# Kernel optimization log

Measured on AMD Instinct MI355X. Metric: run time of the kernel, lower is better.

Reference implementation:

```python
import jax, jax.numpy as jnp
import numpy as np

B, Q, K, D, H = 4, 2048, 2048, 512, 8
DH = D // H
MASK_VAL = -1e6


def setup_inputs() -> dict:
    key = jax.random.key(0)
    ks = jax.random.split(key, 8)
    queries = jax.random.normal(ks[0], (B, Q, D), dtype=jnp.float32)
    keys = jax.random.normal(ks[1], (B, K, D), dtype=jnp.float32)
    values = jax.random.normal(ks[2], (B, K, D), dtype=jnp.float32)
    valid_lens = jax.random.randint(ks[3], (B,), 1, K + 1, dtype=jnp.int32)
    # torch nn.Linear weights: shape [out_features, in_features], y = x @ W.T
    s = 1.0 / np.sqrt(D)
    W_q = jax.random.uniform(ks[4], (D, D), jnp.float32, -s, s)
    W_k = jax.random.uniform(ks[5], (D, D), jnp.float32, -s, s)
    W_v = jax.random.uniform(ks[6], (D, D), jnp.float32, -s, s)
    W_o = jax.random.uniform(ks[7], (D, D), jnp.float32, -s, s)
    return {"queries": queries, "keys": keys, "values": values,
            "valid_lens": valid_lens, "W_q": W_q, "W_k": W_k,
            "W_v": W_v, "W_o": W_o}


def _split_heads(x):
    # [B, S, D] -> [B, H, S, DH]
    b, s, _ = x.shape
    return x.reshape(b, s, H, DH).transpose(0, 2, 1, 3)


def reference(queries, keys, values, valid_lens, W_q, W_k, W_v, W_o):
    q = _split_heads(queries @ W_q.T)   # [B,H,Q,DH]
    k = _split_heads(keys @ W_k.T)      # [B,H,K,DH]
    v = _split_heads(values @ W_v.T)    # [B,H,K,DH]
    scores = jnp.einsum("bhqd,bhkd->bhqk", q, k) / jnp.sqrt(jnp.float32(DH))
    # padding mask: key position < valid_len[b], broadcast over heads & queries
    mask = jnp.arange(K)[None, None, None, :] < valid_lens[:, None, None, None]
    scores = jnp.where(mask, scores, MASK_VAL)
    attn = jax.nn.softmax(scores, axis=-1)  # dropout=eval/no-op
    out = jnp.einsum("bhqk,bhkd->bhqd", attn, v)
    out = out.transpose(0, 2, 1, 3).reshape(queries.shape[0], q.shape[2], D)
    return out @ W_o.T
```

## Files before the change

### kernel.cpp

```cpp
#include <hip/hip_runtime.h>
#include <cstdint>
#include <cstddef>

#define BB  4
#define QQ  2048
#define SK  2048
#define DD  512
#define HH  8
#define DHH 64
#define CS  16
#define ZMAX 2

typedef __bf16 bf16;
typedef bf16  bf16x8 __attribute__((ext_vector_type(8)));
typedef bf16  bf16x4 __attribute__((ext_vector_type(4)));
typedef float f32x4  __attribute__((ext_vector_type(4)));
typedef uint32_t u32x4 __attribute__((ext_vector_type(4)));
typedef _Float16 f16;
typedef f16   f16x4 __attribute__((ext_vector_type(4)));
typedef f16   f16x8 __attribute__((ext_vector_type(8)));

__device__ __forceinline__ void async16(void* lds, const void* g) {
  __builtin_amdgcn_global_load_lds(
      (const __attribute__((address_space(1))) unsigned int*)g,
      (__attribute__((address_space(3))) unsigned int*)lds, 16, 0, 0);
}

__device__ __forceinline__ uint32_t pk2(float lo, float hi) {
  return __builtin_amdgcn_perm(__builtin_bit_cast(uint32_t, hi),
                               __builtin_bit_cast(uint32_t, lo), 0x07060302u);
}

__global__ __launch_bounds__(256) void cvt_all(
    const float* __restrict__ q, const float* __restrict__ k,
    const float* __restrict__ v, const float* __restrict__ w0,
    const float* __restrict__ w1, const float* __restrict__ w2,
    const float* __restrict__ w3, bf16* __restrict__ dq,
    bf16* __restrict__ dk, bf16* __restrict__ dv, bf16* __restrict__ dw0,
    bf16* __restrict__ dw1, bf16* __restrict__ dw2, bf16* __restrict__ dw3,
    int nx4, int nw4) {
  int i = blockIdx.x * 256 + threadIdx.x;
  const float* s;
  bf16* d;
  if (i < nx4)               { s = q;  d = dq;  }
  else if (i < 2 * nx4)      { s = k;  d = dk;  i -= nx4; }
  else if (i < 3 * nx4)      { s = v;  d = dv;  i -= 2 * nx4; }
  else {
    int j = i - 3 * nx4;
    if (j < nw4)             { s = w0; d = dw0; }
    else if (j < 2 * nw4)    { s = w1; d = dw1; j -= nw4; }
    else if (j < 3 * nw4)    { s = w2; d = dw2; j -= 2 * nw4; }
    else if (j < 4 * nw4)    { s = w3; d = dw3; j -= 3 * nw4; }
    else return;
    i = j;
  }
  float4 vv = ((const float4*)s)[i];
  bf16x4 o;
  o[0] = (bf16)vv.x; o[1] = (bf16)vv.y; o[2] = (bf16)vv.z; o[3] = (bf16)vv.w;
  ((bf16x4*)d)[i] = o;
}

template <int MT, typename EpiF>
__device__ __forceinline__ void gemm_body(
    const bf16* __restrict__ A, const bf16* __restrict__ B,
    int tM, int tN, EpiF epi_fn) {
  __shared__ __align__(16) bf16 lA[MT * 32 * 64];
  __shared__ __align__(16) bf16 lB[128 * 64];
  const int tid  = threadIdx.x;
  const int l    = tid & 63;
  const int w    = tid >> 6;
  const int lrow = l & 15, lq = l >> 4;
  const int wm = (w >> 1) * (MT * 16), wn = (w & 1) * 64;

  f32x4 acc[MT][4] = {};
  for (int it = 0; it < 8; ++it) {
    const int kt = it * 64;
    if (it) __syncthreads();
#pragma unroll
    for (int j = 0; j < MT; ++j) {
      int c = j * 256 + tid, row = c >> 3, gcc = (c & 7) ^ (row & 7);
      async16(&lA[c * 8], &A[(size_t)(tM + row) * DD + kt + gcc * 8]);
    }
#pragma unroll
    for (int j = 0; j < 4; ++j) {
      int c = j * 256 + tid, row = c >> 3, gcc = (c & 7) ^ (row & 7);
      async16(&lB[c * 8], &B[(size_t)(tN + row) * DD + kt + gcc * 8]);
    }
    __syncthreads();

#pragma unroll
    for (int ks = 0; ks < 2; ++ks) {
      bf16x8 af[MT], bfr[4];
#pragma unroll
      for (int mt = 0; mt < MT; ++mt) {
        int row = wm + mt * 16 + lrow;
        int chunk = row * 8 + ((ks * 4 + lq) ^ (lrow & 7));
        af[mt] = *(const bf16x8*)&lA[chunk * 8];
      }
#pragma unroll
      for (int nt = 0; nt < 4; ++nt) {
        int row = wn + nt * 16 + lrow;
        int chunk = row * 8 + ((ks * 4 + lq) ^ (lrow & 7));
        bfr[nt] = *(const bf16x8*)&lB[chunk * 8];
      }
#pragma unroll
      for (int mt = 0; mt < MT; ++mt)
#pragma unroll
        for (int nt = 0; nt < 4; ++nt)
          acc[mt][nt] = __builtin_amdgcn_mfma_f32_16x16x32_bf16(
              af[mt], bfr[nt], acc[mt][nt], 0, 0, 0);
    }
  }

#pragma unroll
  for (int mt = 0; mt < MT; ++mt)
#pragma unroll
    for (int nt = 0; nt < 4; ++nt) {
      int row0 = tM + wm + mt * 16 + lq * 4;
      int col  = tN + wn + nt * 16 + lrow;
      epi_fn(acc[mt][nt], row0, col);
    }
}

__global__ __launch_bounds__(256, 3) void proj3(
    const bf16* __restrict__ xq, const bf16* __restrict__ wq, bf16* __restrict__ qh,
    const bf16* __restrict__ xk, const bf16* __restrict__ wk, bf16* __restrict__ kh,
    const bf16* __restrict__ xv, const bf16* __restrict__ wv, bf16* __restrict__ vt,
    float qscale) {
  const int z = blockIdx.y, x = blockIdx.x;
  if (z < 2) {
    const bf16* A  = z == 0 ? wq : wk;
    const bf16* B  = z == 0 ? xq : xk;
    bf16* Cout     = z == 0 ? qh : kh;
    const float scale = z == 0 ? qscale : 1.0f;
    int tM = (x & 3) * 128, tN = (x >> 2) * 128;
    gemm_body<4>(A, B, tM, tN, [&](const f32x4& a, int row0, int col) {
      int b2 = col >> 11, s = col & 2047;
      int h2 = row0 >> 6, dh0 = row0 & 63;
      bf16x4 o;
#pragma unroll
      for (int r = 0; r < 4; ++r) o[r] = (bf16)(a[r] * scale);
      *(bf16x4*)&Cout[((size_t)(b2 * HH + h2) * QQ + s) * DHH + dh0] = o;
    });
  } else {
    int tM = (x >> 2) * 128, tN = (x & 3) * 128;
    gemm_body<4>(xv, wv, tM, tN, [&](const f32x4& a, int row0, int col) {
      int b2 = row0 >> 11, s0 = row0 & 2047;
      int h2 = col >> 6,  dh = col & 63;
      int tile = s0 >> 6, kk = s0 & 63;
      int g = kk >> 4, a2 = (kk >> 2) & 3;
      int idx0 = ((g >> 1) * 4 + a2) * 8 + (g & 1) * 4;
      bf16x4 o;
#pragma unroll
      for (int r = 0; r < 4; ++r) o[r] = (bf16)a[r];
      *(bf16x4*)&vt[((size_t)(b2 * HH + h2) * DHH + dh) * SK + tile * 64 + idx0] = o;
    });
  }
}

__global__ __launch_bounds__(256, 3) void proj_o(
    const bf16* __restrict__ wo, const bf16* __restrict__ ao,
    float* __restrict__ Cout) {
  const int x = blockIdx.x;
  int tM = (x & 7) * 64, tN = (x >> 3) * 128;
  gemm_body<2>(wo, ao, tM, tN, [&](const f32x4& a, int row0, int col) {
    *(float4*)&Cout[(size_t)col * DD + row0] = *(const float4*)&a;
  });
}

__global__ __launch_bounds__(256, 3) void attn_split(
    const bf16* __restrict__ qh, const bf16* __restrict__ kh,
    const bf16* __restrict__ vt, const int* __restrict__ valid_lens,
    f16* __restrict__ opart, float* __restrict__ lpart) {
  __shared__ __align__(16) bf16 lK[3][64 * 64];
  __shared__ __align__(16) bf16 lV[3][64 * 64];
  const int tid  = threadIdx.x;
  const int l    = tid & 63;
  const int w    = tid >> 6;
  const int lrow = l & 15, lq = l >> 4;
  const int rx   = lrow & 7;
  const int bh = blockIdx.x;
  const int b = bh >> 3;
  const int qt = blockIdx.y, z = blockIdx.z;
  const int vl  = valid_lens[b];
  const int nkt = (vl + 63) >> 6;
  const int kt0 = z * CS;
  const int kt1 = min(nkt, kt0 + CS);
  const size_t pbase = ((size_t)bh * 16 + qt) * ZMAX + z;
  float* lout = lpart + pbase * 128;
  f16*   oout = opart + pbase * 8192;

  if (kt0 >= kt1) {
    if (tid < 128) lout[tid] = 0.f;
    return;
  }

  const int q0 = qt * 128 + w * 32;
  const bf16* qbase = qh + (size_t)bh * QQ * DHH;
  const bf16* kbase = kh + (size_t)bh * SK * DHH;
  const bf16* vbase = vt + (size_t)bh * DHH * SK;

  auto stageKV = [&](int k0, int buf) {
#pragma unroll
    for (int j = 0; j < 2; ++j) {
      int c = j * 256 + tid, row = c >> 3, gcc = (c & 7) ^ (row & 7);
      async16(&lK[buf][c * 8], &kbase[(size_t)(k0 + row) * DHH + gcc * 8]);
    }
#pragma unroll
    for (int j = 0; j < 2; ++j) {
      int c = j * 256 + tid, row = c >> 3, gcc = (c & 7) ^ (row & 7);
      async16(&lV[buf][c * 8], &vbase[(size_t)row * SK + k0 + gcc * 8]);
    }
  };

  bf16x8 qf[2][2];
#pragma unroll
  for (int g = 0; g < 2; ++g)
#pragma unroll
    for (int ks = 0; ks < 2; ++ks)
      qf[g][ks] = *(const bf16x8*)
          &qbase[(size_t)(q0 + g * 16 + lrow) * DHH + ks * 32 + lq * 8];

  f32x4 acc[2][4] = {};
  float rs[2] = {0.f, 0.f};

  stageKV(kt0 * 64, 0);
  asm volatile("s_waitcnt vmcnt(0)" ::: "memory");

  for (int kt = kt0; kt < kt1; ++kt) {
    const int bi = (kt - kt0) % 3;
    if (kt + 1 < kt1) {
      stageKV((kt + 1) * 64, (kt + 1 - kt0) % 3);
      asm volatile("s_waitcnt vmcnt(4)" ::: "memory");
    } else {
      asm volatile("s_waitcnt vmcnt(0)" ::: "memory");
    }
    __builtin_amdgcn_s_barrier();
    asm volatile("" ::: "memory");
    const bf16* bufK = lK[bi];
    const bf16* bufV = lV[bi];
    const int k0 = kt * 64;

    f32x4 s[2][4] = {};
#pragma unroll
    for (int ks = 0; ks < 2; ++ks) {
#pragma unroll
      for (int t = 0; t < 4; ++t) {
        int row = t * 16 + lrow;
        int chunkc = row * 8 + ((ks * 4 + lq) ^ rx);
        bf16x8 kf = *(const bf16x8*)&bufK[chunkc * 8];
#pragma unroll
        for (int g = 0; g < 2; ++g)
          s[g][t] = __builtin_amdgcn_mfma_f32_16x16x32_bf16(
              kf, qf[g][ks], s[g][t], 0, 0, 0);
      }
    }

    if (vl < k0 + 64) {
#pragma unroll
      for (int t = 0; t < 4; ++t) {
        int kb = k0 + t * 16 + lq * 4;
#pragma unroll
        for (int r = 0; r < 4; ++r)
          if (kb + r >= vl) { s[0][t][r] = -1e30f; s[1][t][r] = -1e30f; }
      }
    }

#pragma unroll
    for (int g = 0; g < 2; ++g)
#pragma unroll
      for (int t = 0; t < 4; ++t)
#pragma unroll
        for (int r = 0; r < 4; ++r) {
          float p = __builtin_amdgcn_exp2f(s[g][t][r]);
          rs[g] += p;
          s[g][t][r] = p;
        }

#pragma unroll
    for (int p2 = 0; p2 < 2; ++p2) {
      u32x4 pu[2];
#pragma unroll
      for (int g = 0; g < 2; ++g) {
        pu[g][0] = pk2(s[g][2 * p2][0], s[g][2 * p2][1]);
        pu[g][1] = pk2(s[g][2 * p2][2], s[g][2 * p2][3]);
        pu[g][2] = pk2(s[g][2 * p2 + 1][0], s[g][2 * p2 + 1][1]);
        pu[g][3] = pk2(s[g][2 * p2 + 1][2], s[g][2 * p2 + 1][3]);
      }
      bf16x8 pb0 = __builtin_bit_cast(bf16x8, pu[0]);
      bf16x8 pb1 = __builtin_bit_cast(bf16x8, pu[1]);
      int cc = (p2 * 4 + lq) ^ rx;
#pragma unroll
      for (int mt = 0; mt < 4; ++mt) {
        int row = mt * 16 + lrow;
        bf16x8 vf = *(const bf16x8*)&bufV[(row * 8 + cc) * 8];
        acc[0][mt] = __builtin_amdgcn_mfma_f32_16x16x32_bf16(
            vf, pb0, acc[0][mt], 0, 0, 0);
        acc[1][mt] = __builtin_amdgcn_mfma_f32_16x16x32_bf16(
            vf, pb1, acc[1][mt], 0, 0, 0);
      }
    }
  }

#pragma unroll
  for (int g = 0; g < 2; ++g) {
    rs[g] += __shfl_xor(rs[g], 16);
    rs[g] += __shfl_xor(rs[g], 32);
    if (lq == 0) lout[w * 32 + g * 16 + lrow] = rs[g];
  }

#pragma unroll
  for (int g = 0; g < 2; ++g)
#pragma unroll
    for (int mt = 0; mt < 4; ++mt) {
      f16x4 o;
#pragma unroll
      for (int r = 0; r < 4; ++r) o[r] = (f16)acc[g][mt][r];
      *(f16x4*)&oout[(w * 32 + g * 16 + lrow) * 64 + mt * 16 + lq * 4] = o;
    }
}

__global__ __launch_bounds__(256) void attn_combine(
    const f16* __restrict__ opart, const float* __restrict__ lpart,
    bf16* __restrict__ ao) {
  const int bh = blockIdx.x, qt = blockIdx.y;
  const int b = bh >> 3, h = bh & 7;
  const size_t base = ((size_t)bh * 16 + qt) * ZMAX;
  const int t = threadIdx.x, q = t >> 1, ds = (t & 1) * 32;
  float O[32] = {};
  float lsum = 0.f;
#pragma unroll
  for (int z = 0; z < ZMAX; ++z) {
    float lz = lpart[(base + z) * 128 + q];
    if (lz != 0.f) {
      lsum += lz;
      const f16x8* p = (const f16x8*)&opart[(base + z) * 8192 + q * 64 + ds];
#pragma unroll
      for (int j = 0; j < 4; ++j) {
        f16x8 a = p[j];
#pragma unroll
        for (int r = 0; r < 8; ++r) O[j * 8 + r] += (float)a[r];
      }
    }
  }
  float inv = 1.0f / lsum;
  bf16* dst = &ao[((size_t)(b * QQ + qt * 128 + q)) * DD + h * DHH + ds];
#pragma unroll
  for (int j = 0; j < 4; ++j) {
    bf16x8 o;
#pragma unroll
    for (int r = 0; r < 8; ++r) o[r] = (bf16)(O[j * 8 + r] * inv);
    *(bf16x8*)(dst + j * 8) = o;
  }
}

extern "C" void kernel_launch(void* const* d_in, const int* in_sizes, int n_in,
                              void* d_out, int out_size, void* d_ws, size_t ws_size,
                              hipStream_t stream) {
  const float* queries    = (const float*)d_in[0];
  const float* keys       = (const float*)d_in[1];
  const float* values     = (const float*)d_in[2];
  const int*   valid_lens = (const int*)d_in[3];
  const float* W_q = (const float*)d_in[4];
  const float* W_k = (const float*)d_in[5];
  const float* W_v = (const float*)d_in[6];
  const float* W_o = (const float*)d_in[7];

  const size_t NX = (size_t)BB * QQ * DD;
  const size_t NW = (size_t)DD * DD;

  bf16* xq = (bf16*)d_ws;
  bf16* xk = xq + NX;
  bf16* xv = xk + NX;
  bf16* wq = xv + NX;
  bf16* wk = wq + NW;
  bf16* wv = wk + NW;
  bf16* wo = wv + NW;
  bf16* qh = wo + NW;
  bf16* kh = qh + NX;
  bf16* vt = kh + NX;
  f16*  opart = (f16*)(vt + NX);
  float* lpart = (float*)(opart + (size_t)32 * 16 * ZMAX * 8192);
  bf16* ao = xq;

  dim3 blk(256);
  const int nx4 = (int)(NX / 4), nw4 = (int)(NW / 4);
  const int ncvt = (3 * nx4 + 4 * nw4 + 255) / 256;
  cvt_all<<<dim3(ncvt), blk, 0, stream>>>(
      queries, keys, values, W_q, W_k, W_v, W_o,
      xq, xk, xv, wq, wk, wv, wo, nx4, nw4);

  const float qscale = 0.125f * 1.44269504088896340736f;
  proj3<<<dim3(256, 3), blk, 0, stream>>>(xq, wq, qh, xk, wk, kh, xv, wv, vt,
                                          qscale);

  attn_split<<<dim3(BB * HH, QQ / 128, ZMAX), blk, 0, stream>>>(
      qh, kh, vt, valid_lens, opart, lpart);
  attn_combine<<<dim3(BB * HH, QQ / 128), blk, 0, stream>>>(opart, lpart, ao);

  proj_o<<<dim3(512), blk, 0, stream>>>(wo, ao, (float*)d_out);
}
```

Before: 182.1 us.

## Drop split-K attention and combine kernel; fuse normalization into single attention pass

Removes the two-way split over key chunks and the separate combine kernel, so each block walks all valid key tiles and writes the normalized bf16 output directly. This eliminates the fp16 partial output and row-sum traffic plus one kernel launch. In exchange the grid shrinks from 1024 to 512 blocks, which lowers parallelism and can leave the GPU underfilled when valid lengths are long.

```diff
diff --git a/kernel.cpp b/kernel.cpp
--- a/kernel.cpp
+++ b/kernel.cpp
@@ -8,17 +8,12 @@
 #define DD  512
 #define HH  8
 #define DHH 64
-#define CS  16
-#define ZMAX 2
 
 typedef __bf16 bf16;
 typedef bf16  bf16x8 __attribute__((ext_vector_type(8)));
 typedef bf16  bf16x4 __attribute__((ext_vector_type(4)));
 typedef float f32x4  __attribute__((ext_vector_type(4)));
 typedef uint32_t u32x4 __attribute__((ext_vector_type(4)));
-typedef _Float16 f16;
-typedef f16   f16x4 __attribute__((ext_vector_type(4)));
-typedef f16   f16x8 __attribute__((ext_vector_type(8)));
 
 __device__ __forceinline__ void async16(void* lds, const void* g) {
   __builtin_amdgcn_global_load_lds(
@@ -168,10 +163,10 @@
   });
 }
 
-__global__ __launch_bounds__(256, 3) void attn_split(
+__global__ __launch_bounds__(256, 3) void attn_fused(
     const bf16* __restrict__ qh, const bf16* __restrict__ kh,
     const bf16* __restrict__ vt, const int* __restrict__ valid_lens,
-    f16* __restrict__ opart, float* __restrict__ lpart) {
+    bf16* __restrict__ ao) {
   __shared__ __align__(16) bf16 lK[3][64 * 64];
   __shared__ __align__(16) bf16 lV[3][64 * 64];
   const int tid  = threadIdx.x;
@@ -180,20 +175,10 @@
   const int lrow = l & 15, lq = l >> 4;
   const int rx   = lrow & 7;
   const int bh = blockIdx.x;
-  const int b = bh >> 3;
-  const int qt = blockIdx.y, z = blockIdx.z;
+  const int b = bh >> 3, h = bh & 7;
+  const int qt = blockIdx.y;
   const int vl  = valid_lens[b];
   const int nkt = (vl + 63) >> 6;
-  const int kt0 = z * CS;
-  const int kt1 = min(nkt, kt0 + CS);
-  const size_t pbase = ((size_t)bh * 16 + qt) * ZMAX + z;
-  float* lout = lpart + pbase * 128;
-  f16*   oout = opart + pbase * 8192;
-
-  if (kt0 >= kt1) {
-    if (tid < 128) lout[tid] = 0.f;
-    return;
-  }
 
   const int q0 = qt * 128 + w * 32;
   const bf16* qbase = qh + (size_t)bh * QQ * DHH;
@@ -224,13 +209,13 @@
   f32x4 acc[2][4] = {};
   float rs[2] = {0.f, 0.f};
 
-  stageKV(kt0 * 64, 0);
+  stageKV(0, 0);
   asm volatile("s_waitcnt vmcnt(0)" ::: "memory");
 
-  for (int kt = kt0; kt < kt1; ++kt) {
-    const int bi = (kt - kt0) % 3;
-    if (kt + 1 < kt1) {
-      stageKV((kt + 1) * 64, (kt + 1 - kt0) % 3);
+  for (int kt = 0; kt < nkt; ++kt) {
+    const int bi = kt % 3;
+    if (kt + 1 < nkt) {
+      stageKV((kt + 1) * 64, (kt + 1) % 3);
       asm volatile("s_waitcnt vmcnt(4)" ::: "memory");
     } else {
       asm volatile("s_waitcnt vmcnt(0)" ::: "memory");
@@ -306,51 +291,19 @@
   for (int g = 0; g < 2; ++g) {
     rs[g] += __shfl_xor(rs[g], 16);
     rs[g] += __shfl_xor(rs[g], 32);
-    if (lq == 0) lout[w * 32 + g * 16 + lrow] = rs[g];
-  }
-
-#pragma unroll
-  for (int g = 0; g < 2; ++g)
+  }
+
+#pragma unroll
+  for (int g = 0; g < 2; ++g) {
+    float inv = 1.0f / rs[g];
+    int q = q0 + g * 16 + lrow;
 #pragma unroll
     for (int mt = 0; mt < 4; ++mt) {
-      f16x4 o;
-#pragma unroll
-      for (int r = 0; r < 4; ++r) o[r] = (f16)acc[g][mt][r];
-      *(f16x4*)&oout[(w * 32 + g * 16 + lrow) * 64 + mt * 16 + lq * 4] = o;
-    }
-}
-
-__global__ __launch_bounds__(256) void attn_combine(
-    const f16* __restrict__ opart, const float* __restrict__ lpart,
-    bf16* __restrict__ ao) {
-  const int bh = blockIdx.x, qt = blockIdx.y;
-  const int b = bh >> 3, h = bh & 7;
-  const size_t base = ((size_t)bh * 16 + qt) * ZMAX;
-  const int t = threadIdx.x, q = t >> 1, ds = (t & 1) * 32;
-  float O[32] = {};
-  float lsum = 0.f;
-#pragma unroll
-  for (int z = 0; z < ZMAX; ++z) {
-    float lz = lpart[(base + z) * 128 + q];
-    if (lz != 0.f) {
-      lsum += lz;
-      const f16x8* p = (const f16x8*)&opart[(base + z) * 8192 + q * 64 + ds];
-#pragma unroll
-      for (int j = 0; j < 4; ++j) {
-        f16x8 a = p[j];
-#pragma unroll
-        for (int r = 0; r < 8; ++r) O[j * 8 + r] += (float)a[r];
-      }
-    }
-  }
-  float inv = 1.0f / lsum;
-  bf16* dst = &ao[((size_t)(b * QQ + qt * 128 + q)) * DD + h * DHH + ds];
-#pragma unroll
-  for (int j = 0; j < 4; ++j) {
-    bf16x8 o;
-#pragma unroll
-    for (int r = 0; r < 8; ++r) o[r] = (bf16)(O[j * 8 + r] * inv);
-    *(bf16x8*)(dst + j * 8) = o;
+      bf16x4 o;
+#pragma unroll
+      for (int r = 0; r < 4; ++r) o[r] = (bf16)(acc[g][mt][r] * inv);
+      *(bf16x4*)&ao[((size_t)(b * QQ + q)) * DD + h * DHH + mt * 16 + lq * 4] = o;
+    }
   }
 }
 
@@ -379,8 +332,6 @@
   bf16* qh = wo + NW;
   bf16* kh = qh + NX;
   bf16* vt = kh + NX;
-  f16*  opart = (f16*)(vt + NX);
-  float* lpart = (float*)(opart + (size_t)32 * 16 * ZMAX * 8192);
   bf16* ao = xq;
 
   dim3 blk(256);
@@ -394,9 +345,8 @@
   proj3<<<dim3(256, 3), blk, 0, stream>>>(xq, wq, qh, xk, wk, kh, xv, wv, vt,
                                           qscale);
 
-  attn_split<<<dim3(BB * HH, QQ / 128, ZMAX), blk, 0, stream>>>(
-      qh, kh, vt, valid_lens, opart, lpart);
-  attn_combine<<<dim3(BB * HH, QQ / 128), blk, 0, stream>>>(opart, lpart, ao);
+  attn_fused<<<dim3(BB * HH, QQ / 128), blk, 0, stream>>>(
+      qh, kh, vt, valid_lens, ao);
 
   proj_o<<<dim3(512), blk, 0, stream>>>(wo, ao, (float*)d_out);
 }
```

Measured after the change: 175.9 us. -3.4%, faster.
